# Kernel optimization log

Measured on AMD Instinct MI355X. Metric: run time of the kernel, lower is better.

Reference implementation:

```python
import jax, jax.numpy as jnp
import numpy as np

TAU = 18.0


def smooth_compose(X, M, tau=TAU):
    # Z[n,i,j] = smooth_min(X[n,i], M[i,j]) = -(1/tau) * log(exp(-tau*X) + exp(-tau*M))
    # Y[n,j]   = (1/tau) * logsumexp(tau * Z[n,:,j], axis over i)
    # tau*Z = -logaddexp(-tau*X, -tau*M)  (numerically stable, same math)
    tZ = -jnp.logaddexp(-tau * X[:, :, None], -tau * M[None, :, :])  # [n, d, d]
    return (1.0 / tau) * jax.nn.logsumexp(tZ, axis=1)  # [n, d]


def setup_inputs() -> dict:
    key = jax.random.key(0)
    k1, k2, k3, k4, k5 = jax.random.split(key, 5)
    n, p, d = 2048, 1024, 256
    S = jax.random.uniform(k1, (n, p), dtype=jnp.float32)
    T = jax.random.uniform(k2, (n, p), dtype=jnp.float32)
    # learned parameters (A0/M0/B0 defaults are 0.5-filled; use random values of similar scale)
    A = jax.random.uniform(k3, (p, d), dtype=jnp.float32)
    # rawM = logit(M0); random small logits -> M = sigmoid(rawM) near 0.5
    rawM = 0.5 * jax.random.normal(k4, (d, d), dtype=jnp.float32)
    B = jax.random.uniform(k5, (d, p), dtype=jnp.float32)
    return {"S": S, "T": T, "A": A, "rawM": rawM, "B": B}


def reference(S, T, A, rawM, B):
    M = jax.nn.sigmoid(rawM)            # [d, d]
    X_hat = S @ A                       # [n, d]
    Y_hat = T @ A                       # [n, d]
    X_box = jnp.clip(X_hat, 0.0, 1.0)
    Y_box = jnp.clip(Y_hat, 0.0, 1.0)
    Y_pred = smooth_compose(X_box, M, tau=TAU)  # [n, d]
    S_rec = X_hat @ B                   # [n, p]
    T_rec = Y_hat @ B                   # [n, p]
    T_pred = Y_pred @ B                 # [n, p]
    return (X_hat, Y_hat, X_box, Y_box, Y_pred, S_rec, T_rec, T_pred)
```

## Files before the change

### kernel.cpp

```cpp
#include <hip/hip_runtime.h>
#include <math.h>

constexpr int N = 2048;
constexpr int P = 1024;
constexpr int D = 256;
constexpr float TAU = 18.0f;

constexpr size_t OFF_XHAT  = 0;
constexpr size_t OFF_YHAT  = (size_t)N * D;
constexpr size_t OFF_XBOX  = 2 * (size_t)N * D;
constexpr size_t OFF_YBOX  = 3 * (size_t)N * D;
constexpr size_t OFF_YPRED = 4 * (size_t)N * D;
constexpr size_t OFF_SREC  = 5 * (size_t)N * D;

constexpr size_t WS_ATH = 0;
constexpr size_t WS_ATL = 524288;
constexpr size_t WS_BTH = 1048576;
constexpr size_t WS_BTL = 1572864;
constexpr size_t WS_V   = 2097152;
constexpr size_t WS_U   = 2359296;
constexpr size_t WS_LHH = 4456448;
constexpr size_t WS_LHL = 7602176;

typedef short bhalf8 __attribute__((ext_vector_type(8)));
typedef float f32x4  __attribute__((ext_vector_type(4)));

__device__ inline short f2bf(float f) {
  union { float f; unsigned u; } x; x.f = f;
  unsigned r = (x.u + 0x7FFFu + ((x.u >> 16) & 1u)) >> 16;
  return (short)r;
}
__device__ inline float bf2f(short h) {
  union { unsigned u; float f; } x; x.u = ((unsigned)(unsigned short)h) << 16;
  return x.f;
}

__global__ __launch_bounds__(256) void prep_v_kernel(
    const float* __restrict__ rawM, float* __restrict__ V) {
  const int idx = (blockIdx.x * 256 + threadIdx.x) * 4;
  float4 x = *(const float4*)(rawM + idx);
  float4 o;
  o.x = expf(-TAU / (1.0f + expf(-x.x)));
  o.y = expf(-TAU / (1.0f + expf(-x.y)));
  o.z = expf(-TAU / (1.0f + expf(-x.z)));
  o.w = expf(-TAU / (1.0f + expf(-x.w)));
  *(float4*)(V + idx) = o;
}

__global__ __launch_bounds__(256) void transpose_hilo_kernel(
    const float* __restrict__ src, short* __restrict__ dh,
    short* __restrict__ dl, int R, int C) {
  __shared__ __align__(16) float tile[32][36];
  const int t = threadIdx.x;
  const int r0 = blockIdx.x * 32, c0 = blockIdx.y * 32;
  {
    const int tr = t >> 3, tc4 = (t & 7) * 4;
    float4 x = *(const float4*)(src + (size_t)(r0 + tr) * C + c0 + tc4);
    *(float4*)&tile[tr][tc4] = x;
  }
  __syncthreads();
  {
    const int tc = t >> 3, tr4 = (t & 7) * 4;
    short4 h, l;
    float f0 = tile[tr4 + 0][tc];
    float f1 = tile[tr4 + 1][tc];
    float f2 = tile[tr4 + 2][tc];
    float f3 = tile[tr4 + 3][tc];
    h.x = f2bf(f0); l.x = f2bf(f0 - bf2f(h.x));
    h.y = f2bf(f1); l.y = f2bf(f1 - bf2f(h.y));
    h.z = f2bf(f2); l.z = f2bf(f2 - bf2f(h.z));
    h.w = f2bf(f3); l.w = f2bf(f3 - bf2f(h.w));
    *(short4*)(dh + (size_t)(c0 + tc) * R + r0 + tr4) = h;
    *(short4*)(dl + (size_t)(c0 + tc) * R + r0 + tr4) = l;
  }
}

__global__ __launch_bounds__(512) void gemm1_mfma(
    const float* __restrict__ S, const float* __restrict__ Tm,
    const short* __restrict__ Ath, const short* __restrict__ Atl,
    float* __restrict__ out, float* __restrict__ U,
    short* __restrict__ LHh, short* __restrict__ LHl) {
  __shared__ __align__(16) short As_h[2][64][40];
  __shared__ __align__(16) short As_l[2][64][40];
  __shared__ __align__(16) short Bs_h[2][64][40];
  __shared__ __align__(16) short Bs_l[2][64][40];

  const int t  = threadIdx.x;
  const int m0 = blockIdx.x * 64, n0 = blockIdx.y * 64;

  const int srow = t >> 3;
  const int sk   = (t & 7) * 4;
  const int grow = m0 + srow;
  const float* Lrow = (grow < N) ? (S + (size_t)grow * P)
                                 : (Tm + (size_t)(grow - N) * P);
  const short* BhR = Ath + (size_t)(n0 + srow) * P;
  const short* BlR = Atl + (size_t)(n0 + srow) * P;

  const int l = t & 63, w = t >> 6;
  const int wr = (w & 3) * 16, wc = (w >> 2) * 32;
  const int fr = l & 15, ko8 = (l >> 4) * 8, rq = (l >> 4) * 4;

  f32x4 acc[2];
  acc[0] = (f32x4){0.f, 0.f, 0.f, 0.f};
  acc[1] = (f32x4){0.f, 0.f, 0.f, 0.f};

  float4 pa  = *(const float4*)(Lrow + sk);
  short4 pbh = *(const short4*)(BhR + sk);
  short4 pbl = *(const short4*)(BlR + sk);

#define STAGE1(buf)                                        \
  do {                                                     \
    short4 ah4, al4;                                       \
    ah4.x = f2bf(pa.x); al4.x = f2bf(pa.x - bf2f(ah4.x));  \
    ah4.y = f2bf(pa.y); al4.y = f2bf(pa.y - bf2f(ah4.y));  \
    ah4.z = f2bf(pa.z); al4.z = f2bf(pa.z - bf2f(ah4.z));  \
    ah4.w = f2bf(pa.w); al4.w = f2bf(pa.w - bf2f(ah4.w));  \
    *(short4*)&As_h[buf][srow][sk] = ah4;                  \
    *(short4*)&As_l[buf][srow][sk] = al4;                  \
    *(short4*)&Bs_h[buf][srow][sk] = pbh;                  \
    *(short4*)&Bs_l[buf][srow][sk] = pbl;                  \
  } while (0)

  STAGE1(0);

  for (int ks = 0; ks < 32; ++ks) {
    const int b = ks & 1;
    if (ks < 31) {
      const int kn = (ks + 1) * 32;
      pa  = *(const float4*)(Lrow + kn + sk);
      pbh = *(const short4*)(BhR + kn + sk);
      pbl = *(const short4*)(BlR + kn + sk);
    }
    __syncthreads();
    bhalf8 ahv = *(const bhalf8*)&As_h[b][wr + fr][ko8];
    bhalf8 alv = *(const bhalf8*)&As_l[b][wr + fr][ko8];
#pragma unroll
    for (int ni = 0; ni < 2; ++ni) {
      bhalf8 bhv = *(const bhalf8*)&Bs_h[b][wc + ni * 16 + fr][ko8];
      bhalf8 blv = *(const bhalf8*)&Bs_l[b][wc + ni * 16 + fr][ko8];
      acc[ni] = __builtin_amdgcn_mfma_f32_16x16x32_bf16(ahv, bhv, acc[ni], 0, 0, 0);
      acc[ni] = __builtin_amdgcn_mfma_f32_16x16x32_bf16(ahv, blv, acc[ni], 0, 0, 0);
      acc[ni] = __builtin_amdgcn_mfma_f32_16x16x32_bf16(alv, bhv, acc[ni], 0, 0, 0);
    }
    if (ks < 31) STAGE1((ks + 1) & 1);
  }
#undef STAGE1

#pragma unroll
  for (int ni = 0; ni < 2; ++ni) {
    const int col = n0 + wc + ni * 16 + fr;
#pragma unroll
    for (int r = 0; r < 4; ++r) {
      const int row = m0 + wr + rq + r;
      const float v = acc[ni][r];
      const float c = fminf(fmaxf(v, 0.0f), 1.0f);
      const short h  = f2bf(v);
      const short lo = f2bf(v - bf2f(h));
      LHh[(size_t)row * D + col] = h;
      LHl[(size_t)row * D + col] = lo;
      if (row < N) {
        out[OFF_XHAT + (size_t)row * D + col] = v;
        out[OFF_XBOX + (size_t)row * D + col] = c;
        U[(size_t)row * D + col] = expf(-TAU * c);
      } else {
        const size_t ry = (size_t)(row - N);
        out[OFF_YHAT + ry * D + col] = v;
        out[OFF_YBOX + ry * D + col] = c;
      }
    }
  }
}

__global__ __launch_bounds__(256) void smooth_kernel(
    const float* __restrict__ U, const float* __restrict__ V,
    float* __restrict__ ypred, short* __restrict__ LHh,
    short* __restrict__ LHl) {
  __shared__ float us[256][34];
  const int t = threadIdx.x;
  const int n0 = blockIdx.x * 32, j0 = blockIdx.y * 32;

  {
    const int sr = t & 31;
    const int si = (t >> 5) * 32;
    const float* up = U + (size_t)(n0 + sr) * D + si;
#pragma unroll
    for (int q = 0; q < 32; q += 4) {
      float4 x = *(const float4*)(up + q);
      us[si + q + 0][sr] = x.x;
      us[si + q + 1][sr] = x.y;
      us[si + q + 2][sr] = x.z;
      us[si + q + 3][sr] = x.w;
    }
  }
  __syncthreads();

  const int jg = (t & 15) * 2;
  const int nn = (t >> 4) * 2;
  const float* vp = V + j0 + jg;

  float acc00 = 0.f, acc01 = 0.f, acc10 = 0.f, acc11 = 0.f;
#pragma unroll 8
  for (int i = 0; i < D; ++i) {
    float2 u2 = *(const float2*)&us[i][nn];
    float2 v2 = *(const float2*)(vp + (size_t)i * D);
    acc00 += __builtin_amdgcn_rcpf(u2.x + v2.x);
    acc01 += __builtin_amdgcn_rcpf(u2.x + v2.y);
    acc10 += __builtin_amdgcn_rcpf(u2.y + v2.x);
    acc11 += __builtin_amdgcn_rcpf(u2.y + v2.y);
  }

  float a[2][2] = {{acc00, acc01}, {acc10, acc11}};
#pragma unroll
  for (int pI = 0; pI < 2; ++pI) {
    const int row = n0 + nn + pI;
    float2 o;
    o.x = (1.0f / TAU) * logf(a[pI][0]);
    o.y = (1.0f / TAU) * logf(a[pI][1]);
    *(float2*)(ypred + (size_t)row * D + j0 + jg) = o;
    short2 h2, l2;
    h2.x = f2bf(o.x); l2.x = f2bf(o.x - bf2f(h2.x));
    h2.y = f2bf(o.y); l2.y = f2bf(o.y - bf2f(h2.y));
    const size_t lrow = (size_t)(2 * N + row) * D + j0 + jg;
    *(short2*)(LHh + lrow) = h2;
    *(short2*)(LHl + lrow) = l2;
  }
}

__global__ __launch_bounds__(512) void gemm2_mfma(
    const short* __restrict__ LHh, const short* __restrict__ LHl,
    const short* __restrict__ Bth, const short* __restrict__ Btl,
    float* __restrict__ rec) {
  __shared__ __align__(16) short As_h[2][64][40];
  __shared__ __align__(16) short As_l[2][64][40];
  __shared__ __align__(16) short Bs_h[2][64][40];
  __shared__ __align__(16) short Bs_l[2][64][40];

  const int t  = threadIdx.x;
  const int m0 = blockIdx.x * 64, n0 = blockIdx.y * 64;

  const int srow = t >> 3;
  const int sk   = (t & 7) * 4;
  const short* AhR = LHh + (size_t)(m0 + srow) * D;
  const short* AlR = LHl + (size_t)(m0 + srow) * D;
  const short* BhR = Bth + (size_t)(n0 + srow) * D;
  const short* BlR = Btl + (size_t)(n0 + srow) * D;

  const int l = t & 63, w = t >> 6;
  const int wr = (w & 3) * 16, wc = (w >> 2) * 32;
  const int fr = l & 15, ko8 = (l >> 4) * 8, rq = (l >> 4) * 4;

  f32x4 acc[2];
  acc[0] = (f32x4){0.f, 0.f, 0.f, 0.f};
  acc[1] = (f32x4){0.f, 0.f, 0.f, 0.f};

  short4 pah = *(const short4*)(AhR + sk);
  short4 pal = *(const short4*)(AlR + sk);
  short4 pbh = *(const short4*)(BhR + sk);
  short4 pbl = *(const short4*)(BlR + sk);

#define STAGE2(buf)                            \
  do {                                         \
    *(short4*)&As_h[buf][srow][sk] = pah;      \
    *(short4*)&As_l[buf][srow][sk] = pal;      \
    *(short4*)&Bs_h[buf][srow][sk] = pbh;      \
    *(short4*)&Bs_l[buf][srow][sk] = pbl;      \
  } while (0)

  STAGE2(0);

  for (int ks = 0; ks < 8; ++ks) {
    const int b = ks & 1;
    if (ks < 7) {
      const int kn = (ks + 1) * 32;
      pah = *(const short4*)(AhR + kn + sk);
      pal = *(const short4*)(AlR + kn + sk);
      pbh = *(const short4*)(BhR + kn + sk);
      pbl = *(const short4*)(BlR + kn + sk);
    }
    __syncthreads();
    bhalf8 ahv = *(const bhalf8*)&As_h[b][wr + fr][ko8];
    bhalf8 alv = *(const bhalf8*)&As_l[b][wr + fr][ko8];
#pragma unroll
    for (int ni = 0; ni < 2; ++ni) {
      bhalf8 bhv = *(const bhalf8*)&Bs_h[b][wc + ni * 16 + fr][ko8];
      bhalf8 blv = *(const bhalf8*)&Bs_l[b][wc + ni * 16 + fr][ko8];
      acc[ni] = __builtin_amdgcn_mfma_f32_16x16x32_bf16(ahv, bhv, acc[ni], 0, 0, 0);
      acc[ni] = __builtin_amdgcn_mfma_f32_16x16x32_bf16(ahv, blv, acc[ni], 0, 0, 0);
      acc[ni] = __builtin_amdgcn_mfma_f32_16x16x32_bf16(alv, bhv, acc[ni], 0, 0, 0);
    }
    if (ks < 7) STAGE2((ks + 1) & 1);
  }
#undef STAGE2

#pragma unroll
  for (int ni = 0; ni < 2; ++ni) {
    const int col = n0 + wc + ni * 16 + fr;
#pragma unroll
    for (int r = 0; r < 4; ++r) {
      const int row = m0 + wr + rq + r;
      rec[(size_t)row * P + col] = acc[ni][r];
    }
  }
}

extern "C" void kernel_launch(void* const* d_in, const int* in_sizes, int n_in,
                              void* d_out, int out_size, void* d_ws,
                              size_t ws_size, hipStream_t stream) {
  const float* S    = (const float*)d_in[0];
  const float* T    = (const float*)d_in[1];
  const float* A    = (const float*)d_in[2];
  const float* rawM = (const float*)d_in[3];
  const float* B    = (const float*)d_in[4];
  float* out = (float*)d_out;
  char* ws = (char*)d_ws;

  short* Ath = (short*)(ws + WS_ATH);
  short* Atl = (short*)(ws + WS_ATL);
  short* Bth = (short*)(ws + WS_BTH);
  short* Btl = (short*)(ws + WS_BTL);
  float* V   = (float*)(ws + WS_V);
  float* U   = (float*)(ws + WS_U);
  short* LHh = (short*)(ws + WS_LHH);
  short* LHl = (short*)(ws + WS_LHL);

  prep_v_kernel<<<64, 256, 0, stream>>>(rawM, V);
  transpose_hilo_kernel<<<dim3(32, 8), 256, 0, stream>>>(A, Ath, Atl, P, D);
  transpose_hilo_kernel<<<dim3(8, 32), 256, 0, stream>>>(B, Bth, Btl, D, P);
  gemm1_mfma<<<dim3(64, 4), 512, 0, stream>>>(S, T, Ath, Atl, out, U, LHh, LHl);
  smooth_kernel<<<dim3(64, 8), 256, 0, stream>>>(U, V, out + OFF_YPRED, LHh, LHl);
  gemm2_mfma<<<dim3(96, 16), 512, 0, stream>>>(LHh, LHl, Bth, Btl, out + OFF_SREC);
}
```

Baseline: 138.7 us.

## Merge prep kernels and retile all GEMM and smooth kernels for occupancy

Folds the sigmoid/exp prep and both hi/lo transposes into a single launch, removing two kernel launches. gemm1 moves to 256-thread blocks with 32-row tiles, doubling the grid. The smooth kernel uses 16-row tiles, also doubling its grid. gemm2 gives each wave a 2x2 MFMA tile with wider 8-element loads for more reuse per LDS read. Together these trade per-block reuse for more blocks and fewer launches; the smaller gemm1 tile re-reads A more often.

Result: slower. 148.3 us (+6.9%).

```diff
diff --git a/kernel.cpp b/kernel.cpp
--- a/kernel.cpp
+++ b/kernel.cpp
@@ -35,24 +35,11 @@
   return x.f;
 }
 
-__global__ __launch_bounds__(256) void prep_v_kernel(
-    const float* __restrict__ rawM, float* __restrict__ V) {
-  const int idx = (blockIdx.x * 256 + threadIdx.x) * 4;
-  float4 x = *(const float4*)(rawM + idx);
-  float4 o;
-  o.x = expf(-TAU / (1.0f + expf(-x.x)));
-  o.y = expf(-TAU / (1.0f + expf(-x.y)));
-  o.z = expf(-TAU / (1.0f + expf(-x.z)));
-  o.w = expf(-TAU / (1.0f + expf(-x.w)));
-  *(float4*)(V + idx) = o;
-}
-
-__global__ __launch_bounds__(256) void transpose_hilo_kernel(
+__device__ inline void transpose_hilo_body(
     const float* __restrict__ src, short* __restrict__ dh,
-    short* __restrict__ dl, int R, int C) {
+    short* __restrict__ dl, int R, int C, int bx, int by, int t) {
   __shared__ __align__(16) float tile[32][36];
-  const int t = threadIdx.x;
-  const int r0 = blockIdx.x * 32, c0 = blockIdx.y * 32;
+  const int r0 = bx * 32, c0 = by * 32;
   {
     const int tr = t >> 3, tc4 = (t & 7) * 4;
     float4 x = *(const float4*)(src + (size_t)(r0 + tr) * C + c0 + tc4);
@@ -75,38 +62,65 @@
   }
 }
 
-__global__ __launch_bounds__(512) void gemm1_mfma(
+__global__ __launch_bounds__(256) void prep_all_kernel(
+    const float* __restrict__ A, const float* __restrict__ rawM,
+    const float* __restrict__ B, short* __restrict__ Ath,
+    short* __restrict__ Atl, short* __restrict__ Bth,
+    short* __restrict__ Btl, float* __restrict__ V) {
+  const int bid = blockIdx.x;
+  const int t = threadIdx.x;
+  if (bid < 64) {
+    const int idx = (bid * 256 + t) * 4;
+    float4 x = *(const float4*)(rawM + idx);
+    float4 o;
+    o.x = expf(-TAU / (1.0f + expf(-x.x)));
+    o.y = expf(-TAU / (1.0f + expf(-x.y)));
+    o.z = expf(-TAU / (1.0f + expf(-x.z)));
+    o.w = expf(-TAU / (1.0f + expf(-x.w)));
+    *(float4*)(V + idx) = o;
+  } else if (bid < 320) {
+    const int idx = bid - 64;
+    transpose_hilo_body(A, Ath, Atl, P, D, idx & 31, idx >> 5, t);
+  } else {
+    const int idx = bid - 320;
+    transpose_hilo_body(B, Bth, Btl, D, P, idx & 7, idx >> 3, t);
+  }
+}
+
+__global__ __launch_bounds__(256) void gemm1_mfma(
     const float* __restrict__ S, const float* __restrict__ Tm,
     const short* __restrict__ Ath, const short* __restrict__ Atl,
     float* __restrict__ out, float* __restrict__ U,
     short* __restrict__ LHh, short* __restrict__ LHl) {
-  __shared__ __align__(16) short As_h[2][64][40];
-  __shared__ __align__(16) short As_l[2][64][40];
+  __shared__ __align__(16) short As_h[2][32][40];
+  __shared__ __align__(16) short As_l[2][32][40];
   __shared__ __align__(16) short Bs_h[2][64][40];
   __shared__ __align__(16) short Bs_l[2][64][40];
 
   const int t  = threadIdx.x;
-  const int m0 = blockIdx.x * 64, n0 = blockIdx.y * 64;
-
-  const int srow = t >> 3;
-  const int sk   = (t & 7) * 4;
-  const int grow = m0 + srow;
+  const int m0 = blockIdx.x * 32, n0 = blockIdx.y * 64;
+
+  const int arow = t >> 3;
+  const int ak   = (t & 7) * 4;
+  const int grow = m0 + arow;
   const float* Lrow = (grow < N) ? (S + (size_t)grow * P)
                                  : (Tm + (size_t)(grow - N) * P);
-  const short* BhR = Ath + (size_t)(n0 + srow) * P;
-  const short* BlR = Atl + (size_t)(n0 + srow) * P;
+  const int brow = t >> 2;
+  const int bk   = (t & 3) * 8;
+  const short* BhR = Ath + (size_t)(n0 + brow) * P;
+  const short* BlR = Atl + (size_t)(n0 + brow) * P;
 
   const int l = t & 63, w = t >> 6;
-  const int wr = (w & 3) * 16, wc = (w >> 2) * 32;
+  const int wr = (w & 1) * 16, wc = (w >> 1) * 32;
   const int fr = l & 15, ko8 = (l >> 4) * 8, rq = (l >> 4) * 4;
 
   f32x4 acc[2];
   acc[0] = (f32x4){0.f, 0.f, 0.f, 0.f};
   acc[1] = (f32x4){0.f, 0.f, 0.f, 0.f};
 
-  float4 pa  = *(const float4*)(Lrow + sk);
-  short4 pbh = *(const short4*)(BhR + sk);
-  short4 pbl = *(const short4*)(BlR + sk);
+  float4 pa  = *(const float4*)(Lrow + ak);
+  bhalf8 pbh = *(const bhalf8*)(BhR + bk);
+  bhalf8 pbl = *(const bhalf8*)(BlR + bk);
 
 #define STAGE1(buf)                                        \
   do {                                                     \
@@ -115,10 +129,10 @@
     ah4.y = f2bf(pa.y); al4.y = f2bf(pa.y - bf2f(ah4.y));  \
     ah4.z = f2bf(pa.z); al4.z = f2bf(pa.z - bf2f(ah4.z));  \
     ah4.w = f2bf(pa.w); al4.w = f2bf(pa.w - bf2f(ah4.w));  \
-    *(short4*)&As_h[buf][srow][sk] = ah4;                  \
-    *(short4*)&As_l[buf][srow][sk] = al4;                  \
-    *(short4*)&Bs_h[buf][srow][sk] = pbh;                  \
-    *(short4*)&Bs_l[buf][srow][sk] = pbl;                  \
+    *(short4*)&As_h[buf][arow][ak] = ah4;                  \
+    *(short4*)&As_l[buf][arow][ak] = al4;                  \
+    *(bhalf8*)&Bs_h[buf][brow][bk] = pbh;                  \
+    *(bhalf8*)&Bs_l[buf][brow][bk] = pbl;                  \
   } while (0)
 
   STAGE1(0);
@@ -127,9 +141,9 @@
     const int b = ks & 1;
     if (ks < 31) {
       const int kn = (ks + 1) * 32;
-      pa  = *(const float4*)(Lrow + kn + sk);
-      pbh = *(const short4*)(BhR + kn + sk);
-      pbl = *(const short4*)(BlR + kn + sk);
+      pa  = *(const float4*)(Lrow + kn + ak);
+      pbh = *(const bhalf8*)(BhR + kn + bk);
+      pbl = *(const bhalf8*)(BlR + kn + bk);
     }
     __syncthreads();
     bhalf8 ahv = *(const bhalf8*)&As_h[b][wr + fr][ko8];
@@ -175,16 +189,16 @@
     const float* __restrict__ U, const float* __restrict__ V,
     float* __restrict__ ypred, short* __restrict__ LHh,
     short* __restrict__ LHl) {
-  __shared__ float us[256][34];
+  __shared__ float us[256][17];
   const int t = threadIdx.x;
-  const int n0 = blockIdx.x * 32, j0 = blockIdx.y * 32;
+  const int n0 = blockIdx.x * 16, j0 = blockIdx.y * 32;
 
   {
-    const int sr = t & 31;
-    const int si = (t >> 5) * 32;
+    const int sr = t & 15;
+    const int si = (t >> 4) * 16;
     const float* up = U + (size_t)(n0 + sr) * D + si;
 #pragma unroll
-    for (int q = 0; q < 32; q += 4) {
+    for (int q = 0; q < 16; q += 4) {
       float4 x = *(const float4*)(up + q);
       us[si + q + 0][sr] = x.x;
       us[si + q + 1][sr] = x.y;
@@ -195,38 +209,32 @@
   __syncthreads();
 
   const int jg = (t & 15) * 2;
-  const int nn = (t >> 4) * 2;
+  const int nn = t >> 4;
   const float* vp = V + j0 + jg;
 
-  float acc00 = 0.f, acc01 = 0.f, acc10 = 0.f, acc11 = 0.f;
+  float acc0 = 0.f, acc1 = 0.f;
 #pragma unroll 8
   for (int i = 0; i < D; ++i) {
-    float2 u2 = *(const float2*)&us[i][nn];
+    const float u = us[i][nn];
     float2 v2 = *(const float2*)(vp + (size_t)i * D);
-    acc00 += __builtin_amdgcn_rcpf(u2.x + v2.x);
-    acc01 += __builtin_amdgcn_rcpf(u2.x + v2.y);
-    acc10 += __builtin_amdgcn_rcpf(u2.y + v2.x);
-    acc11 += __builtin_amdgcn_rcpf(u2.y + v2.y);
-  }
-
-  float a[2][2] = {{acc00, acc01}, {acc10, acc11}};
-#pragma unroll
-  for (int pI = 0; pI < 2; ++pI) {
-    const int row = n0 + nn + pI;
-    float2 o;
-    o.x = (1.0f / TAU) * logf(a[pI][0]);
-    o.y = (1.0f / TAU) * logf(a[pI][1]);
-    *(float2*)(ypred + (size_t)row * D + j0 + jg) = o;
-    short2 h2, l2;
-    h2.x = f2bf(o.x); l2.x = f2bf(o.x - bf2f(h2.x));
-    h2.y = f2bf(o.y); l2.y = f2bf(o.y - bf2f(h2.y));
-    const size_t lrow = (size_t)(2 * N + row) * D + j0 + jg;
-    *(short2*)(LHh + lrow) = h2;
-    *(short2*)(LHl + lrow) = l2;
-  }
-}
-
-__global__ __launch_bounds__(512) void gemm2_mfma(
+    acc0 += __builtin_amdgcn_rcpf(u + v2.x);
+    acc1 += __builtin_amdgcn_rcpf(u + v2.y);
+  }
+
+  const int row = n0 + nn;
+  float2 o;
+  o.x = (1.0f / TAU) * logf(acc0);
+  o.y = (1.0f / TAU) * logf(acc1);
+  *(float2*)(ypred + (size_t)row * D + j0 + jg) = o;
+  short2 h2, l2;
+  h2.x = f2bf(o.x); l2.x = f2bf(o.x - bf2f(h2.x));
+  h2.y = f2bf(o.y); l2.y = f2bf(o.y - bf2f(h2.y));
+  const size_t lrow = (size_t)(2 * N + row) * D + j0 + jg;
+  *(short2*)(LHh + lrow) = h2;
+  *(short2*)(LHl + lrow) = l2;
+}
+
+__global__ __launch_bounds__(256) void gemm2_mfma(
     const short* __restrict__ LHh, const short* __restrict__ LHl,
     const short* __restrict__ Bth, const short* __restrict__ Btl,
     float* __restrict__ rec) {
@@ -238,32 +246,34 @@
   const int t  = threadIdx.x;
   const int m0 = blockIdx.x * 64, n0 = blockIdx.y * 64;
 
-  const int srow = t >> 3;
-  const int sk   = (t & 7) * 4;
+  const int srow = t >> 2;
+  const int sk   = (t & 3) * 8;
   const short* AhR = LHh + (size_t)(m0 + srow) * D;
   const short* AlR = LHl + (size_t)(m0 + srow) * D;
   const short* BhR = Bth + (size_t)(n0 + srow) * D;
   const short* BlR = Btl + (size_t)(n0 + srow) * D;
 
   const int l = t & 63, w = t >> 6;
-  const int wr = (w & 3) * 16, wc = (w >> 2) * 32;
+  const int wr = (w & 1) * 32, wc = (w >> 1) * 32;
   const int fr = l & 15, ko8 = (l >> 4) * 8, rq = (l >> 4) * 4;
 
-  f32x4 acc[2];
-  acc[0] = (f32x4){0.f, 0.f, 0.f, 0.f};
-  acc[1] = (f32x4){0.f, 0.f, 0.f, 0.f};
-
-  short4 pah = *(const short4*)(AhR + sk);
-  short4 pal = *(const short4*)(AlR + sk);
-  short4 pbh = *(const short4*)(BhR + sk);
-  short4 pbl = *(const short4*)(BlR + sk);
+  f32x4 acc[2][2];
+#pragma unroll
+  for (int i = 0; i < 2; ++i)
+#pragma unroll
+    for (int j = 0; j < 2; ++j) acc[i][j] = (f32x4){0.f, 0.f, 0.f, 0.f};
+
+  bhalf8 pah = *(const bhalf8*)(AhR + sk);
+  bhalf8 pal = *(const bhalf8*)(AlR + sk);
+  bhalf8 pbh = *(const bhalf8*)(BhR + sk);
+  bhalf8 pbl = *(const bhalf8*)(BlR + sk);
 
 #define STAGE2(buf)                            \
   do {                                         \
-    *(short4*)&As_h[buf][srow][sk] = pah;      \
-    *(short4*)&As_l[buf][srow][sk] = pal;      \
-    *(short4*)&Bs_h[buf][srow][sk] = pbh;      \
-    *(short4*)&Bs_l[buf][srow][sk] = pbl;      \
+    *(bhalf8*)&As_h[buf][srow][sk] = pah;      \
+    *(bhalf8*)&As_l[buf][srow][sk] = pal;      \
+    *(bhalf8*)&Bs_h[buf][srow][sk] = pbh;      \
+    *(bhalf8*)&Bs_l[buf][srow][sk] = pbl;      \
   } while (0)
 
   STAGE2(0);
@@ -272,35 +282,43 @@
     const int b = ks & 1;
     if (ks < 7) {
       const int kn = (ks + 1) * 32;
-      pah = *(const short4*)(AhR + kn + sk);
-      pal = *(const short4*)(AlR + kn + sk);
-      pbh = *(const short4*)(BhR + kn + sk);
-      pbl = *(const short4*)(BlR + kn + sk);
+      pah = *(const bhalf8*)(AhR + kn + sk);
+      pal = *(const bhalf8*)(AlR + kn + sk);
+      pbh = *(const bhalf8*)(BhR + kn + sk);
+      pbl = *(const bhalf8*)(BlR + kn + sk);
     }
     __syncthreads();
-    bhalf8 ahv = *(const bhalf8*)&As_h[b][wr + fr][ko8];
-    bhalf8 alv = *(const bhalf8*)&As_l[b][wr + fr][ko8];
+    bhalf8 ahv[2], alv[2], bhv[2], blv[2];
+#pragma unroll
+    for (int mi = 0; mi < 2; ++mi) {
+      ahv[mi] = *(const bhalf8*)&As_h[b][wr + mi * 16 + fr][ko8];
+      alv[mi] = *(const bhalf8*)&As_l[b][wr + mi * 16 + fr][ko8];
+      bhv[mi] = *(const bhalf8*)&Bs_h[b][wc + mi * 16 + fr][ko8];
+      blv[mi] = *(const bhalf8*)&Bs_l[b][wc + mi * 16 + fr][ko8];
+    }
+#pragma unroll
+    for (int mi = 0; mi < 2; ++mi)
+#pragma unroll
+      for (int ni = 0; ni < 2; ++ni) {
+        acc[mi][ni] = __builtin_amdgcn_mfma_f32_16x16x32_bf16(ahv[mi], bhv[ni], acc[mi][ni], 0, 0, 0);
+        acc[mi][ni] = __builtin_amdgcn_mfma_f32_16x16x32_bf16(ahv[mi], blv[ni], acc[mi][ni], 0, 0, 0);
+        acc[mi][ni] = __builtin_amdgcn_mfma_f32_16x16x32_bf16(alv[mi], bhv[ni], acc[mi][ni], 0, 0, 0);
+      }
+    if (ks < 7) STAGE2((ks + 1) & 1);
+  }
+#undef STAGE2
+
+#pragma unroll
+  for (int mi = 0; mi < 2; ++mi)
 #pragma unroll
     for (int ni = 0; ni < 2; ++ni) {
-      bhalf8 bhv = *(const bhalf8*)&Bs_h[b][wc + ni * 16 + fr][ko8];
-      bhalf8 blv = *(const bhalf8*)&Bs_l[b][wc + ni * 16 + fr][ko8];
-      acc[ni] = __builtin_amdgcn_mfma_f32_16x16x32_bf16(ahv, bhv, acc[ni], 0, 0, 0);
-      acc[ni] = __builtin_amdgcn_mfma_f32_16x16x32_bf16(ahv, blv, acc[ni], 0, 0, 0);
-      acc[ni] = __builtin_amdgcn_mfma_f32_16x16x32_bf16(alv, bhv, acc[ni], 0, 0, 0);
-    }
-    if (ks < 7) STAGE2((ks + 1) & 1);
-  }
-#undef STAGE2
-
-#pragma unroll
-  for (int ni = 0; ni < 2; ++ni) {
-    const int col = n0 + wc + ni * 16 + fr;
-#pragma unroll
-    for (int r = 0; r < 4; ++r) {
-      const int row = m0 + wr + rq + r;
-      rec[(size_t)row * P + col] = acc[ni][r];
-    }
-  }
+      const int col = n0 + wc + ni * 16 + fr;
+#pragma unroll
+      for (int r = 0; r < 4; ++r) {
+        const int row = m0 + wr + mi * 16 + rq + r;
+        rec[(size_t)row * P + col] = acc[mi][ni][r];
+      }
+    }
 }
 
 extern "C" void kernel_launch(void* const* d_in, const int* in_sizes, int n_in,
@@ -323,10 +341,8 @@
   short* LHh = (short*)(ws + WS_LHH);
   short* LHl = (short*)(ws + WS_LHL);
 
-  prep_v_kernel<<<64, 256, 0, stream>>>(rawM, V);
-  transpose_hilo_kernel<<<dim3(32, 8), 256, 0, stream>>>(A, Ath, Atl, P, D);
-  transpose_hilo_kernel<<<dim3(8, 32), 256, 0, stream>>>(B, Bth, Btl, D, P);
-  gemm1_mfma<<<dim3(64, 4), 512, 0, stream>>>(S, T, Ath, Atl, out, U, LHh, LHl);
-  smooth_kernel<<<dim3(64, 8), 256, 0, stream>>>(U, V, out + OFF_YPRED, LHh, LHl);
-  gemm2_mfma<<<dim3(96, 16), 512, 0, stream>>>(LHh, LHl, Bth, Btl, out + OFF_SREC);
-}
+  prep_all_kernel<<<576, 256, 0, stream>>>(A, rawM, B, Ath, Atl, Bth, Btl, V);
+  gemm1_mfma<<<dim3(128, 4), 256, 0, stream>>>(S, T, Ath, Atl, out, U, LHh, LHl);
+  smooth_kernel<<<dim3(128, 8), 256, 0, stream>>>(U, V, out + OFF_YPRED, LHh, LHl);
+  gemm2_mfma<<<dim3(96, 16), 256, 0, stream>>>(LHh, LHl, Bth, Btl, out + OFF_SREC);
+}
```
